# Kernel optimization log

Hardware: AMD Instinct MI355X
Metric: run time of the kernel (lower is better)

Reference implementation:

```python
import jax, jax.numpy as jnp
import numpy as np

S, R, STEPS, EPS = 1, 1, 4, 1e-6

def setup_inputs() -> dict:
    key = jax.random.key(0)
    k1, k2, k3, k4 = jax.random.split(key, 4)
    x = jax.random.normal(k1, (8, 16, 160, 48, 48), dtype=jnp.float32)
    W_pre = jax.random.normal(k2, (8, 16), dtype=jnp.float32) * 0.1   # align conv 1x1x1
    W_post1 = jax.random.normal(k3, (8, 8), dtype=jnp.float32) * 0.1
    W_post2 = jax.random.normal(k4, (16, 8), dtype=jnp.float32) * 0.1
    return {"x": x, "W_pre": W_pre, "W_post1": W_post1, "W_post2": W_post2}

def _update_coef(x3, bases, coef):
    # x3:[B,D,N] bases:[B,D,R] coef:[B,N,R] -- NMF multiplicative coef update
    num = jnp.einsum('bdn,bdr->bnr', x3, bases)
    btb = jnp.einsum('bdr,bdq->brq', bases, bases)
    den = jnp.einsum('bnr,brq->bnq', coef, btb)
    return coef * num / (den + EPS)

def _local_step(x3, bases, coef):
    coef = _update_coef(x3, bases, coef)
    num = jnp.einsum('bdn,bnr->bdr', x3, coef)
    ctc = jnp.einsum('bnr,bnq->brq', coef, coef)
    den = jnp.einsum('bdr,brq->bdq', bases, ctc)
    bases = bases * num / (den + EPS)
    return bases, coef

def _nmf(x3):
    # rand_init bases = normalize(ones, dim=1) = 1/sqrt(D)
    B, D, N = x3.shape
    bases = jnp.full((B, D, R), 1.0 / np.sqrt(float(D)), dtype=x3.dtype)
    def _infer(x3, bases):
        coef = jax.nn.softmax(jnp.einsum('bdn,bdr->bnr', x3, bases), axis=-1)  # inv_t = 1
        for _ in range(STEPS):
            bases, coef = _local_step(x3, bases, coef)
        return bases, coef
    # torch runs local_inference under no_grad
    bases, coef = jax.lax.stop_gradient(_infer(x3, bases))
    coef = _update_coef(x3, bases, coef)  # compute_coef (differentiable)
    return jnp.einsum('bdr,bnr->bdn', bases, coef)  # reconstruction [B,D,N]

def reference(x, W_pre, W_post1, W_post2):
    B, C, T, H, W = x.shape
    # pre 1x1x1 conv (no bias) + ReLU
    h = jax.nn.relu(jnp.einsum('oc,bcthw->bothw', W_pre, x))
    Ca = W_pre.shape[0]
    D, N = T // S, Ca * H * W
    x3 = h.reshape(B * S, D, N)  # flat view, matches torch .view on contiguous [B,Ca,T,H,W]
    recon = _nmf(x3).reshape(B, Ca, T, H, W)
    # post: 1x1x1 conv + ReLU, then 1x1x1 conv (no act)
    y = jax.nn.relu(jnp.einsum('oc,bcthw->bothw', W_post1, recon))
    y = jnp.einsum('oc,bcthw->bothw', W_post2, y)
    return y
```

## Files before the change

### kernel.cpp

```cpp
#include <hip/hip_runtime.h>
#include <math.h>

using u16 = unsigned short;
using u32 = unsigned int;

typedef __attribute__((ext_vector_type(8))) short bf16x8;
typedef __attribute__((ext_vector_type(16))) float f32x16;

constexpr int Bn  = 8;
constexpr int Cin = 16;
constexpr int Tn  = 160;
constexpr int HWn = 2304;
constexpr int Dn  = 160;
constexpr int Nn  = 8 * HWn;
constexpr int PB  = Dn * Nn;
constexpr int PLANE4 = Tn * HWn / 4;
constexpr float EPSF = 1e-6f;
constexpr float B0F  = 0.07905694150420949f;
constexpr float BTB0 = 160.0f * B0F * B0F;

constexpr int NSPLIT = 72;
constexpr int NTRI   = 15;
constexpr int TSZ    = NTRI * 1024;
constexpr int GD     = Dn * Dn;

constexpr size_t G_OFF  = (size_t)Bn * PB / 2;
constexpr size_t GP_OFF = G_OFF + (size_t)Bn * GD;

constexpr int OFF_COEF = 0;
constexpr int OFF_B4   = Bn * Nn;
constexpr int OFF_BTB  = OFF_B4 + Bn * Dn;

__device__ inline float bf2f(u16 u) { return __uint_as_float(((u32)u) << 16); }
__device__ inline u16 f2bf(float f) {
    u32 x = __float_as_uint(f);
    return (u16)((x + 0x7fffu + ((x >> 16) & 1u)) >> 16);
}

__device__ inline void tri_pair(int t, int& a, int& bb) {
    a = (t >= 14) ? 4 : (t >= 12) ? 3 : (t >= 9) ? 2 : (t >= 5) ? 1 : 0;
    int base = (a == 0) ? 0 : (a == 1) ? 5 : (a == 2) ? 9 : (a == 3) ? 12 : 14;
    bb = a + (t - base);
}

__global__ __launch_bounds__(256) void k_pre(const float* __restrict__ x,
                                             const float* __restrict__ Wpre,
                                             u16* __restrict__ h) {
    __shared__ float Ws[8 * Cin];
    if (threadIdx.x < 8 * Cin) Ws[threadIdx.x] = Wpre[threadIdx.x];
    __syncthreads();
    int gid = blockIdx.x * 256 + threadIdx.x;
    int b   = gid / PLANE4;
    int pos = gid - b * PLANE4;
    const float4* xb = reinterpret_cast<const float4*>(x) + (size_t)(b * Cin) * PLANE4 + pos;
    float4 acc[8];
#pragma unroll
    for (int o = 0; o < 8; ++o) acc[o] = make_float4(0.f, 0.f, 0.f, 0.f);
#pragma unroll
    for (int c = 0; c < Cin; ++c) {
        float4 xv = xb[(size_t)c * PLANE4];
#pragma unroll
        for (int o = 0; o < 8; ++o) {
            float w = Ws[o * Cin + c];
            acc[o].x = fmaf(w, xv.x, acc[o].x);
            acc[o].y = fmaf(w, xv.y, acc[o].y);
            acc[o].z = fmaf(w, xv.z, acc[o].z);
            acc[o].w = fmaf(w, xv.w, acc[o].w);
        }
    }
#pragma unroll
    for (int o = 0; o < 8; ++o) {
        float4 v = acc[o];
        u32 w0 = (u32)f2bf(fmaxf(v.x, 0.f)) | ((u32)f2bf(fmaxf(v.y, 0.f)) << 16);
        u32 w1 = (u32)f2bf(fmaxf(v.z, 0.f)) | ((u32)f2bf(fmaxf(v.w, 0.f)) << 16);
        uint2* dst = reinterpret_cast<uint2*>(h + (size_t)(b * 8 + o) * (Tn * HWn)) + pos;
        *dst = make_uint2(w0, w1);
    }
}

__global__ __launch_bounds__(256, 3) void k_gram(const u16* __restrict__ h,
                                                 float* __restrict__ Gpart) {
    __shared__ uint4 tile[Dn * 16];
    const int blk = blockIdx.x;
    const int b = blk / NSPLIT, s = blk - b * NSPLIT;
    const int tid = threadIdx.x;
    const int w = tid >> 6, l = tid & 63, lo = l & 31, hi = l >> 5;
    const int c8 = tid & 15, rg = tid >> 4;
    const int swl = lo & 7;

    int a0, b0_, a1, b1_, a2, b2_, a3, b3_;
    tri_pair(w,      a0, b0_);
    tri_pair(w + 4,  a1, b1_);
    tri_pair(w + 8,  a2, b2_);
    const bool has3 = (w < 3);
    tri_pair(has3 ? (w + 12) : 0, a3, b3_);
    const int rA0 = a0 * 32, rB0 = b0_ * 32, dg0 = (a0 == b0_);
    const int rA1 = a1 * 32, rB1 = b1_ * 32, dg1 = (a1 == b1_);
    const int rA2 = a2 * 32, rB2 = b2_ * 32, dg2 = (a2 == b2_);
    const int rA3 = a3 * 32, rB3 = b3_ * 32, dg3 = (a3 == b3_);

    f32x16 acc0, acc1, acc2, acc3;
#pragma unroll
    for (int q = 0; q < 16; ++q) { acc0[q] = 0.f; acc1[q] = 0.f; acc2[q] = 0.f; acc3[q] = 0.f; }

    const u16* hb = h + (size_t)b * PB;
#pragma unroll 1
    for (int cc = 0; cc < 2; ++cc) {
        const int kbase = (s * 2 + cc) * 128;
        __syncthreads();
#pragma unroll
        for (int k = 0; k < 10; ++k) {
            int row = rg + 16 * k;
            uint4 v = *reinterpret_cast<const uint4*>(
                hb + (size_t)row * Nn + kbase + c8 * 8);
            tile[row * 16 + (c8 ^ (row & 7))] = v;
        }
        __syncthreads();
#pragma unroll
        for (int kk = 0; kk < 8; ++kk) {
            const int sw = (kk * 2 + hi) ^ swl;
            bf16x8 fa0 = __builtin_bit_cast(bf16x8, tile[(rA0 + lo) * 16 + sw]);
            bf16x8 fb0 = dg0 ? fa0 : __builtin_bit_cast(bf16x8, tile[(rB0 + lo) * 16 + sw]);
            acc0 = __builtin_amdgcn_mfma_f32_32x32x16_bf16(fa0, fb0, acc0, 0, 0, 0);
            bf16x8 fa1 = __builtin_bit_cast(bf16x8, tile[(rA1 + lo) * 16 + sw]);
            bf16x8 fb1 = dg1 ? fa1 : __builtin_bit_cast(bf16x8, tile[(rB1 + lo) * 16 + sw]);
            acc1 = __builtin_amdgcn_mfma_f32_32x32x16_bf16(fa1, fb1, acc1, 0, 0, 0);
            bf16x8 fa2 = __builtin_bit_cast(bf16x8, tile[(rA2 + lo) * 16 + sw]);
            bf16x8 fb2 = dg2 ? fa2 : __builtin_bit_cast(bf16x8, tile[(rB2 + lo) * 16 + sw]);
            acc2 = __builtin_amdgcn_mfma_f32_32x32x16_bf16(fa2, fb2, acc2, 0, 0, 0);
            if (has3) {
                bf16x8 fa3 = __builtin_bit_cast(bf16x8, tile[(rA3 + lo) * 16 + sw]);
                bf16x8 fb3 = dg3 ? fa3 : __builtin_bit_cast(bf16x8, tile[(rB3 + lo) * 16 + sw]);
                acc3 = __builtin_amdgcn_mfma_f32_32x32x16_bf16(fa3, fb3, acc3, 0, 0, 0);
            }
        }
    }

    float* Gp = Gpart + (size_t)blk * TSZ;
#pragma unroll
    for (int q = 0; q < 16; ++q) {
        int row = ((q & 3) + 8 * (q >> 2) + 4 * hi) * 32 + lo;
        Gp[(w)      * 1024 + row] = acc0[q];
        Gp[(w + 4)  * 1024 + row] = acc1[q];
        Gp[(w + 8)  * 1024 + row] = acc2[q];
        if (has3) Gp[(w + 12) * 1024 + row] = acc3[q];
    }
}

__global__ __launch_bounds__(256) void k_redG(const float* __restrict__ Gpart,
                                              float* __restrict__ G) {
    int idx = blockIdx.x * 256 + threadIdx.x;
    int b = idx / TSZ;
    int r = idx - b * TSZ;
    int t = r >> 10;
    int e = r & 1023;
    int er = e >> 5, ec = e & 31;
    int a, bb;
    tri_pair(t, a, bb);
    const float* gp = Gpart + (size_t)(b * NSPLIT) * TSZ + r;
    float s = 0.f;
#pragma unroll 8
    for (int k = 0; k < NSPLIT; ++k) s += gp[(size_t)k * TSZ];
    float* Gb = G + (size_t)b * GD;
    int i = a * 32 + er, j = bb * 32 + ec;
    Gb[i * Dn + j] = s;
    Gb[j * Dn + i] = s;
}

__global__ __launch_bounds__(192) void k_chainB(const float* __restrict__ G,
                                                float* __restrict__ bases4,
                                                float* __restrict__ btb4) {
    __shared__ float bS[Dn];
    __shared__ float uS[Dn];
    __shared__ float sc[2];
    const int b = blockIdx.x;
    const int tid = threadIdx.x;
    const float* Gb = G + (size_t)b * GD;

    if (tid < Dn) bS[tid] = B0F;
    __syncthreads();

    float btb = BTB0;
#pragma unroll 1
    for (int j = 1; j <= 4; ++j) {
        if (tid < Dn) {
            float s = 0.f;
            const float* row = Gb + tid * Dn;
#pragma unroll 8
            for (int d = 0; d < Dn; ++d) s = fmaf(row[d], bS[d], s);
            uS[tid] = s;
        }
        __syncthreads();
        if (tid == 0) {
            float bgb = 0.f;
            for (int d = 0; d < Dn; ++d) bgb = fmaf(bS[d], uS[d], bgb);
            sc[0] = bgb;
        }
        __syncthreads();
        float denom = (j == 1) ? (btb + EPSF) : btb;
        float ctc = sc[0] / (denom * denom);
        float inv = 1.f / (denom * ctc);
        if (tid < Dn) bS[tid] = uS[tid] * inv;
        __syncthreads();
        if (tid == 0) {
            float ss = 0.f;
            for (int d = 0; d < Dn; ++d) ss = fmaf(bS[d], bS[d], ss);
            sc[1] = ss;
        }
        __syncthreads();
        btb = sc[1];
    }
    if (tid < Dn) bases4[b * Dn + tid] = bS[tid];
    if (tid == 0) btb4[b] = btb;
}

__global__ __launch_bounds__(256, 3) void k_coef5(
        const u16* __restrict__ h, float* __restrict__ coef,
        const float* __restrict__ bases4, const float* __restrict__ btb4)
{
    __shared__ float bsS[Dn];
    __shared__ float partA[4][128];
    const int blk = blockIdx.x;
    const int b   = blk / 144;
    const int cb  = blk - b * 144;
    const int colbase = cb * 128;
    const int tid = threadIdx.x, c8 = tid & 15, rg = tid >> 4;

    if (tid < Dn) bsS[tid] = bases4[b * Dn + tid] / btb4[b];
    __syncthreads();

    const u16* hp = h + (size_t)b * PB + colbase + c8 * 8;
    float acc[8];
#pragma unroll
    for (int j = 0; j < 8; ++j) acc[j] = 0.f;
#pragma unroll
    for (int k = 0; k < 10; ++k) {
        uint4 v = *reinterpret_cast<const uint4*>(hp + (size_t)(rg + 16 * k) * Nn);
        float w = bsS[rg + 16 * k];
        u32 vv[4] = { v.x, v.y, v.z, v.w };
#pragma unroll
        for (int q = 0; q < 4; ++q) {
            acc[2*q]   = fmaf(w, bf2f((u16)(vv[q] & 0xffffu)), acc[2*q]);
            acc[2*q+1] = fmaf(w, bf2f((u16)(vv[q] >> 16)),     acc[2*q+1]);
        }
    }
#pragma unroll
    for (int j = 0; j < 8; ++j) {
        acc[j] += __shfl_xor(acc[j], 16, 64);
        acc[j] += __shfl_xor(acc[j], 32, 64);
    }
    if ((tid & 48) == 0) {
        int w = tid >> 6;
#pragma unroll
        for (int j = 0; j < 8; ++j) partA[w][c8 * 8 + j] = acc[j];
    }
    __syncthreads();

    if (tid < 128)
        coef[(size_t)b * Nn + colbase + tid] =
            partA[0][tid] + partA[1][tid] + partA[2][tid] + partA[3][tid];
}

__global__ __launch_bounds__(192) void k_post(const float* __restrict__ coef,
                                              const float* __restrict__ bases,
                                              const float* __restrict__ Wp1,
                                              const float* __restrict__ Wp2,
                                              float* __restrict__ out) {
    int b = blockIdx.x / Tn;
    int t = blockIdx.x - b * Tn;
    int tau = t >> 3;
    float u[8];
#pragma unroll
    for (int p = 0; p < 8; ++p) {
        float s = 0.f;
#pragma unroll
        for (int ca = 0; ca < 8; ++ca)
            s = fmaf(Wp1[p * 8 + ca], bases[b * Dn + ca * 20 + tau], s);
        u[p] = fmaxf(s, 0.f);
    }
    float v[16];
#pragma unroll
    for (int o = 0; o < 16; ++o) {
        float s = 0.f;
#pragma unroll
        for (int p = 0; p < 8; ++p) s = fmaf(Wp2[o * 8 + p], u[p], s);
        v[o] = s;
    }
    const float4* c4 = reinterpret_cast<const float4*>(coef + (size_t)b * Nn + (t & 7) * HWn);
    float4* o4 = reinterpret_cast<float4*>(out) + (size_t)(b * 16 * Tn + t) * (HWn / 4);
#pragma unroll
    for (int it = 0; it < 3; ++it) {
        int p4 = threadIdx.x + it * 192;
        float4 cv = c4[p4];
#pragma unroll
        for (int o = 0; o < 16; ++o) {
            float4 ov = make_float4(cv.x * v[o], cv.y * v[o], cv.z * v[o], cv.w * v[o]);
            o4[(size_t)o * (Tn * (HWn / 4)) + p4] = ov;
        }
    }
}

extern "C" void kernel_launch(void* const* d_in, const int* in_sizes, int n_in,
                              void* d_out, int out_size, void* d_ws, size_t ws_size,
                              hipStream_t stream) {
    const float* x    = (const float*)d_in[0];
    const float* Wpre = (const float*)d_in[1];
    const float* Wp1  = (const float*)d_in[2];
    const float* Wp2  = (const float*)d_in[3];
    float* out = (float*)d_out;

    u16*   h     = (u16*)d_out;
    float* G     = out + G_OFF;
    float* Gpart = out + GP_OFF;
    float* ws = (float*)d_ws;
    float* coef   = ws + OFF_COEF;
    float* bases4 = ws + OFF_B4;
    float* btb4   = ws + OFF_BTB;

    k_pre<<<Bn * PLANE4 / 256, 256, 0, stream>>>(x, Wpre, h);
    k_gram<<<Bn * NSPLIT, 256, 0, stream>>>(h, Gpart);
    k_redG<<<Bn * TSZ / 256, 256, 0, stream>>>(Gpart, G);
    k_chainB<<<Bn, 192, 0, stream>>>(G, bases4, btb4);
    k_coef5<<<Bn * 144, 256, 0, stream>>>(h, coef, bases4, btb4);
    k_post<<<Bn * Tn, 192, 0, stream>>>(coef, bases4, Wp1, Wp2, out);
}
```

Before: 146.0 us.

## Fuse pre-conv into Gram kernel, computing bf16 tiles directly from x

```diff
diff --git a/kernel.cpp b/kernel.cpp
--- a/kernel.cpp
+++ b/kernel.cpp
@@ -14,12 +14,12 @@
 constexpr int Dn  = 160;
 constexpr int Nn  = 8 * HWn;
 constexpr int PB  = Dn * Nn;
-constexpr int PLANE4 = Tn * HWn / 4;
+constexpr int TH  = Tn * HWn;
 constexpr float EPSF = 1e-6f;
 constexpr float B0F  = 0.07905694150420949f;
 constexpr float BTB0 = 160.0f * B0F * B0F;
 
-constexpr int NSPLIT = 72;
+constexpr int NSPLIT = 36;
 constexpr int NTRI   = 15;
 constexpr int TSZ    = NTRI * 1024;
 constexpr int GD     = Dn * Dn;
@@ -43,50 +43,20 @@
     bb = a + (t - base);
 }
 
-__global__ __launch_bounds__(256) void k_pre(const float* __restrict__ x,
-                                             const float* __restrict__ Wpre,
-                                             u16* __restrict__ h) {
+__global__ __launch_bounds__(256, 2) void k_pregram(
+        const float* __restrict__ x, const float* __restrict__ Wpre,
+        u16* __restrict__ h, float* __restrict__ Gpart) {
+    __shared__ uint4 tile[Dn * 16];
     __shared__ float Ws[8 * Cin];
-    if (threadIdx.x < 8 * Cin) Ws[threadIdx.x] = Wpre[threadIdx.x];
-    __syncthreads();
-    int gid = blockIdx.x * 256 + threadIdx.x;
-    int b   = gid / PLANE4;
-    int pos = gid - b * PLANE4;
-    const float4* xb = reinterpret_cast<const float4*>(x) + (size_t)(b * Cin) * PLANE4 + pos;
-    float4 acc[8];
-#pragma unroll
-    for (int o = 0; o < 8; ++o) acc[o] = make_float4(0.f, 0.f, 0.f, 0.f);
-#pragma unroll
-    for (int c = 0; c < Cin; ++c) {
-        float4 xv = xb[(size_t)c * PLANE4];
-#pragma unroll
-        for (int o = 0; o < 8; ++o) {
-            float w = Ws[o * Cin + c];
-            acc[o].x = fmaf(w, xv.x, acc[o].x);
-            acc[o].y = fmaf(w, xv.y, acc[o].y);
-            acc[o].z = fmaf(w, xv.z, acc[o].z);
-            acc[o].w = fmaf(w, xv.w, acc[o].w);
-        }
-    }
-#pragma unroll
-    for (int o = 0; o < 8; ++o) {
-        float4 v = acc[o];
-        u32 w0 = (u32)f2bf(fmaxf(v.x, 0.f)) | ((u32)f2bf(fmaxf(v.y, 0.f)) << 16);
-        u32 w1 = (u32)f2bf(fmaxf(v.z, 0.f)) | ((u32)f2bf(fmaxf(v.w, 0.f)) << 16);
-        uint2* dst = reinterpret_cast<uint2*>(h + (size_t)(b * 8 + o) * (Tn * HWn)) + pos;
-        *dst = make_uint2(w0, w1);
-    }
-}
-
-__global__ __launch_bounds__(256, 3) void k_gram(const u16* __restrict__ h,
-                                                 float* __restrict__ Gpart) {
-    __shared__ uint4 tile[Dn * 16];
     const int blk = blockIdx.x;
     const int b = blk / NSPLIT, s = blk - b * NSPLIT;
     const int tid = threadIdx.x;
     const int w = tid >> 6, l = tid & 63, lo = l & 31, hi = l >> 5;
-    const int c8 = tid & 15, rg = tid >> 4;
     const int swl = lo & 7;
+    const int cp  = tid & 63;
+    const int tg5 = (tid >> 6) * 5;
+
+    if (tid < 8 * Cin) Ws[tid] = Wpre[tid];
 
     int a0, b0_, a1, b1_, a2, b2_, a3, b3_;
     tri_pair(w,      a0, b0_);
@@ -103,19 +73,57 @@
 #pragma unroll
     for (int q = 0; q < 16; ++q) { acc0[q] = 0.f; acc1[q] = 0.f; acc2[q] = 0.f; acc3[q] = 0.f; }
 
-    const u16* hb = h + (size_t)b * PB;
+    const float* xb = x + (size_t)b * Cin * TH;
+    u16* hb = h + (size_t)b * PB;
+    u32* tw = reinterpret_cast<u32*>(tile);
+    __syncthreads();
+
 #pragma unroll 1
-    for (int cc = 0; cc < 2; ++cc) {
-        const int kbase = (s * 2 + cc) * 128;
-        __syncthreads();
-#pragma unroll
-        for (int k = 0; k < 10; ++k) {
-            int row = rg + 16 * k;
-            uint4 v = *reinterpret_cast<const uint4*>(
-                hb + (size_t)row * Nn + kbase + c8 * 8);
-            tile[row * 16 + (c8 ^ (row & 7))] = v;
-        }
-        __syncthreads();
+    for (int cc = 0; cc < 4; ++cc) {
+        const int kbase = s * 512 + cc * 128;
+        const int r = kbase / HWn;
+        const int hw0 = kbase - r * HWn + 2 * cp;
+        const float* xp = xb + (size_t)r * HWn + hw0;
+
+        float ac[5][16];
+#pragma unroll
+        for (int i = 0; i < 5; ++i)
+#pragma unroll
+            for (int q = 0; q < 16; ++q) ac[i][q] = 0.f;
+
+#pragma unroll 2
+        for (int c = 0; c < Cin; ++c) {
+            float2 xv[5];
+#pragma unroll
+            for (int i = 0; i < 5; ++i)
+                xv[i] = *reinterpret_cast<const float2*>(
+                    xp + (size_t)c * TH + (size_t)((tg5 + i) * 8) * HWn);
+#pragma unroll
+            for (int ca = 0; ca < 8; ++ca) {
+                float wv = Ws[ca * Cin + c];
+#pragma unroll
+                for (int i = 0; i < 5; ++i) {
+                    ac[i][2 * ca]     = fmaf(wv, xv[i].x, ac[i][2 * ca]);
+                    ac[i][2 * ca + 1] = fmaf(wv, xv[i].y, ac[i][2 * ca + 1]);
+                }
+            }
+        }
+
+        __syncthreads();
+#pragma unroll
+        for (int ca = 0; ca < 8; ++ca) {
+#pragma unroll
+            for (int i = 0; i < 5; ++i) {
+                int d = ca * 20 + tg5 + i;
+                u32 pkd = (u32)f2bf(fmaxf(ac[i][2 * ca], 0.f))
+                        | ((u32)f2bf(fmaxf(ac[i][2 * ca + 1], 0.f)) << 16);
+                tw[d * 64 + (((cp >> 2) ^ (d & 7)) << 2) + (cp & 3)] = pkd;
+                *reinterpret_cast<u32*>(hb + (size_t)d * Nn + kbase + 2 * cp) = pkd;
+            }
+        }
+        __syncthreads();
+        __builtin_amdgcn_sched_barrier(0);
+
 #pragma unroll
         for (int kk = 0; kk < 8; ++kk) {
             const int sw = (kk * 2 + hi) ^ swl;
@@ -134,6 +142,7 @@
                 acc3 = __builtin_amdgcn_mfma_f32_32x32x16_bf16(fa3, fb3, acc3, 0, 0, 0);
             }
         }
+        __syncthreads();
     }
 
     float* Gp = Gpart + (size_t)blk * TSZ;
@@ -159,7 +168,7 @@
     tri_pair(t, a, bb);
     const float* gp = Gpart + (size_t)(b * NSPLIT) * TSZ + r;
     float s = 0.f;
-#pragma unroll 8
+#pragma unroll 4
     for (int k = 0; k < NSPLIT; ++k) s += gp[(size_t)k * TSZ];
     float* Gb = G + (size_t)b * GD;
     int i = a * 32 + er, j = bb * 32 + ec;
@@ -317,8 +326,7 @@
     float* bases4 = ws + OFF_B4;
     float* btb4   = ws + OFF_BTB;
 
-    k_pre<<<Bn * PLANE4 / 256, 256, 0, stream>>>(x, Wpre, h);
-    k_gram<<<Bn * NSPLIT, 256, 0, stream>>>(h, Gpart);
+    k_pregram<<<Bn * NSPLIT, 256, 0, stream>>>(x, Wpre, h, Gpart);
     k_redG<<<Bn * TSZ / 256, 256, 0, stream>>>(Gpart, G);
     k_chainB<<<Bn, 192, 0, stream>>>(G, bases4, btb4);
     k_coef5<<<Bn * 144, 256, 0, stream>>>(h, coef, bases4, btb4);
```

Measured after the change: 267.7 us. 83.3% more time.

## Replace Gram partial buffer and reduction kernel with atomic accumulation

Applied to the files above, without the earlier changes.

```diff
diff --git a/kernel.cpp b/kernel.cpp
--- a/kernel.cpp
+++ b/kernel.cpp
@@ -21,11 +21,9 @@
 
 constexpr int NSPLIT = 72;
 constexpr int NTRI   = 15;
-constexpr int TSZ    = NTRI * 1024;
 constexpr int GD     = Dn * Dn;
 
 constexpr size_t G_OFF  = (size_t)Bn * PB / 2;
-constexpr size_t GP_OFF = G_OFF + (size_t)Bn * GD;
 
 constexpr int OFF_COEF = 0;
 constexpr int OFF_B4   = Bn * Nn;
@@ -45,11 +43,15 @@
 
 __global__ __launch_bounds__(256) void k_pre(const float* __restrict__ x,
                                              const float* __restrict__ Wpre,
-                                             u16* __restrict__ h) {
+                                             u16* __restrict__ h,
+                                             float* __restrict__ G) {
     __shared__ float Ws[8 * Cin];
     if (threadIdx.x < 8 * Cin) Ws[threadIdx.x] = Wpre[threadIdx.x];
     __syncthreads();
     int gid = blockIdx.x * 256 + threadIdx.x;
+    if (gid < Bn * GD / 4) {
+        reinterpret_cast<float4*>(G)[gid] = make_float4(0.f, 0.f, 0.f, 0.f);
+    }
     int b   = gid / PLANE4;
     int pos = gid - b * PLANE4;
     const float4* xb = reinterpret_cast<const float4*>(x) + (size_t)(b * Cin) * PLANE4 + pos;
@@ -79,7 +81,7 @@
 }
 
 __global__ __launch_bounds__(256, 3) void k_gram(const u16* __restrict__ h,
-                                                 float* __restrict__ Gpart) {
+                                                 float* __restrict__ G) {
     __shared__ uint4 tile[Dn * 16];
     const int blk = blockIdx.x;
     const int b = blk / NSPLIT, s = blk - b * NSPLIT;
@@ -136,35 +138,15 @@
         }
     }
 
-    float* Gp = Gpart + (size_t)blk * TSZ;
+    float* Gb = G + (size_t)b * GD;
 #pragma unroll
     for (int q = 0; q < 16; ++q) {
-        int row = ((q & 3) + 8 * (q >> 2) + 4 * hi) * 32 + lo;
-        Gp[(w)      * 1024 + row] = acc0[q];
-        Gp[(w + 4)  * 1024 + row] = acc1[q];
-        Gp[(w + 8)  * 1024 + row] = acc2[q];
-        if (has3) Gp[(w + 12) * 1024 + row] = acc3[q];
-    }
-}
-
-__global__ __launch_bounds__(256) void k_redG(const float* __restrict__ Gpart,
-                                              float* __restrict__ G) {
-    int idx = blockIdx.x * 256 + threadIdx.x;
-    int b = idx / TSZ;
-    int r = idx - b * TSZ;
-    int t = r >> 10;
-    int e = r & 1023;
-    int er = e >> 5, ec = e & 31;
-    int a, bb;
-    tri_pair(t, a, bb);
-    const float* gp = Gpart + (size_t)(b * NSPLIT) * TSZ + r;
-    float s = 0.f;
-#pragma unroll 8
-    for (int k = 0; k < NSPLIT; ++k) s += gp[(size_t)k * TSZ];
-    float* Gb = G + (size_t)b * GD;
-    int i = a * 32 + er, j = bb * 32 + ec;
-    Gb[i * Dn + j] = s;
-    Gb[j * Dn + i] = s;
+        int R = (q & 3) + 8 * (q >> 2) + 4 * hi;
+        atomicAdd(&Gb[(a0 * 32 + R) * Dn + b0_ * 32 + lo], acc0[q]);
+        atomicAdd(&Gb[(a1 * 32 + R) * Dn + b1_ * 32 + lo], acc1[q]);
+        atomicAdd(&Gb[(a2 * 32 + R) * Dn + b2_ * 32 + lo], acc2[q]);
+        if (has3) atomicAdd(&Gb[(a3 * 32 + R) * Dn + b3_ * 32 + lo], acc3[q]);
+    }
 }
 
 __global__ __launch_bounds__(192) void k_chainB(const float* __restrict__ G,
@@ -185,9 +167,11 @@
     for (int j = 1; j <= 4; ++j) {
         if (tid < Dn) {
             float s = 0.f;
-            const float* row = Gb + tid * Dn;
 #pragma unroll 8
-            for (int d = 0; d < Dn; ++d) s = fmaf(row[d], bS[d], s);
+            for (int d = 0; d < Dn; ++d) {
+                float g = (tid <= d) ? Gb[tid * Dn + d] : Gb[d * Dn + tid];
+                s = fmaf(g, bS[d], s);
+            }
             uS[tid] = s;
         }
         __syncthreads();
@@ -311,15 +295,13 @@
 
     u16*   h     = (u16*)d_out;
     float* G     = out + G_OFF;
-    float* Gpart = out + GP_OFF;
     float* ws = (float*)d_ws;
     float* coef   = ws + OFF_COEF;
     float* bases4 = ws + OFF_B4;
     float* btb4   = ws + OFF_BTB;
 
-    k_pre<<<Bn * PLANE4 / 256, 256, 0, stream>>>(x, Wpre, h);
-    k_gram<<<Bn * NSPLIT, 256, 0, stream>>>(h, Gpart);
-    k_redG<<<Bn * TSZ / 256, 256, 0, stream>>>(Gpart, G);
+    k_pre<<<Bn * PLANE4 / 256, 256, 0, stream>>>(x, Wpre, h, G);
+    k_gram<<<Bn * NSPLIT, 256, 0, stream>>>(h, G);
     k_chainB<<<Bn, 192, 0, stream>>>(G, bases4, btb4);
     k_coef5<<<Bn * 144, 256, 0, stream>>>(h, coef, bases4, btb4);
     k_post<<<Bn * Tn, 192, 0, stream>>>(coef, bases4, Wp1, Wp2, out);
```

After: 199.3 us. +36.5%, slower.

## Fuse coefficient computation with post convs, moving h to workspace

Applied to the files above, without the earlier changes.

```diff
diff --git a/kernel.cpp b/kernel.cpp
--- a/kernel.cpp
+++ b/kernel.cpp
@@ -27,9 +27,11 @@
 constexpr size_t G_OFF  = (size_t)Bn * PB / 2;
 constexpr size_t GP_OFF = G_OFF + (size_t)Bn * GD;
 
-constexpr int OFF_COEF = 0;
-constexpr int OFF_B4   = Bn * Nn;
+constexpr int OFF_B4   = 0;
 constexpr int OFF_BTB  = OFF_B4 + Bn * Dn;
+constexpr int OFF_COEF = 2048;
+constexpr size_t OFF_H = 151552;
+constexpr size_t WS_NEED_A = (OFF_H + (size_t)Bn * PB / 2) * 4;
 
 __device__ inline float bf2f(u16 u) { return __uint_as_float(((u32)u) << 16); }
 __device__ inline u16 f2bf(float f) {
@@ -300,6 +302,89 @@
     }
 }
 
+__global__ __launch_bounds__(256, 3) void k_cpost(
+        const u16* __restrict__ h,
+        const float* __restrict__ bases4, const float* __restrict__ btb4,
+        const float* __restrict__ Wp1, const float* __restrict__ Wp2,
+        float* __restrict__ out)
+{
+    __shared__ float bsS[Dn];
+    __shared__ float partA[4][128];
+    __shared__ float uS[160];
+    __shared__ float vS[320];
+    __shared__ float cS[128];
+    const int blk = blockIdx.x;
+    const int b   = blk / 144;
+    const int cb  = blk - b * 144;
+    const int colbase = cb * 128;
+    const int r   = cb / 18;
+    const int hw0 = (cb - r * 18) * 128;
+    const int tid = threadIdx.x, c8 = tid & 15, rg = tid >> 4;
+
+    if (tid < Dn) bsS[tid] = bases4[b * Dn + tid] / btb4[b];
+    if (tid < 160) {
+        int p = tid / 20, tau = tid - p * 20;
+        float s = 0.f;
+#pragma unroll
+        for (int ca = 0; ca < 8; ++ca)
+            s = fmaf(Wp1[p * 8 + ca], bases4[b * Dn + ca * 20 + tau], s);
+        uS[tid] = fmaxf(s, 0.f);
+    }
+    __syncthreads();
+
+    for (int i = tid; i < 320; i += 256) {
+        int o = i / 20, tau = i - o * 20;
+        float s = 0.f;
+#pragma unroll
+        for (int p = 0; p < 8; ++p) s = fmaf(Wp2[o * 8 + p], uS[p * 20 + tau], s);
+        vS[i] = s;
+    }
+
+    const u16* hp = h + (size_t)b * PB + colbase + c8 * 8;
+    float acc[8];
+#pragma unroll
+    for (int j = 0; j < 8; ++j) acc[j] = 0.f;
+#pragma unroll
+    for (int k = 0; k < 10; ++k) {
+        uint4 v = *reinterpret_cast<const uint4*>(hp + (size_t)(rg + 16 * k) * Nn);
+        float w = bsS[rg + 16 * k];
+        u32 vv[4] = { v.x, v.y, v.z, v.w };
+#pragma unroll
+        for (int q = 0; q < 4; ++q) {
+            acc[2*q]   = fmaf(w, bf2f((u16)(vv[q] & 0xffffu)), acc[2*q]);
+            acc[2*q+1] = fmaf(w, bf2f((u16)(vv[q] >> 16)),     acc[2*q+1]);
+        }
+    }
+#pragma unroll
+    for (int j = 0; j < 8; ++j) {
+        acc[j] += __shfl_xor(acc[j], 16, 64);
+        acc[j] += __shfl_xor(acc[j], 32, 64);
+    }
+    if ((tid & 48) == 0) {
+        int w = tid >> 6;
+#pragma unroll
+        for (int j = 0; j < 8; ++j) partA[w][c8 * 8 + j] = acc[j];
+    }
+    __syncthreads();
+    if (tid < 128)
+        cS[tid] = partA[0][tid] + partA[1][tid] + partA[2][tid] + partA[3][tid];
+    __syncthreads();
+
+    const int col4 = tid & 31;
+    const int rbase = tid >> 5;
+    float4 c = *reinterpret_cast<const float4*>(&cS[col4 * 4]);
+    float4* o4 = reinterpret_cast<float4*>(out);
+    const size_t base_b = (size_t)(b * 16) * 160 * 576 + (size_t)r * 576 + (hw0 >> 2) + col4;
+#pragma unroll 8
+    for (int k = 0; k < 40; ++k) {
+        int row = rbase + 8 * k;
+        int o = row / 20, tau = row - o * 20;
+        float vv = vS[row];
+        o4[base_b + (size_t)(o * 160 + tau * 8) * 576] =
+            make_float4(c.x * vv, c.y * vv, c.z * vv, c.w * vv);
+    }
+}
+
 extern "C" void kernel_launch(void* const* d_in, const int* in_sizes, int n_in,
                               void* d_out, int out_size, void* d_ws, size_t ws_size,
                               hipStream_t stream) {
@@ -308,19 +393,28 @@
     const float* Wp1  = (const float*)d_in[2];
     const float* Wp2  = (const float*)d_in[3];
     float* out = (float*)d_out;
-
-    u16*   h     = (u16*)d_out;
-    float* G     = out + G_OFF;
-    float* Gpart = out + GP_OFF;
-    float* ws = (float*)d_ws;
-    float* coef   = ws + OFF_COEF;
+    float* ws  = (float*)d_ws;
+
+    float* G      = out + G_OFF;
+    float* Gpart  = out + GP_OFF;
     float* bases4 = ws + OFF_B4;
     float* btb4   = ws + OFF_BTB;
 
-    k_pre<<<Bn * PLANE4 / 256, 256, 0, stream>>>(x, Wpre, h);
-    k_gram<<<Bn * NSPLIT, 256, 0, stream>>>(h, Gpart);
-    k_redG<<<Bn * TSZ / 256, 256, 0, stream>>>(Gpart, G);
-    k_chainB<<<Bn, 192, 0, stream>>>(G, bases4, btb4);
-    k_coef5<<<Bn * 144, 256, 0, stream>>>(h, coef, bases4, btb4);
-    k_post<<<Bn * Tn, 192, 0, stream>>>(coef, bases4, Wp1, Wp2, out);
-}
+    if (ws_size >= WS_NEED_A) {
+        u16* h = (u16*)(ws + OFF_H);
+        k_pre<<<Bn * PLANE4 / 256, 256, 0, stream>>>(x, Wpre, h);
+        k_gram<<<Bn * NSPLIT, 256, 0, stream>>>(h, Gpart);
+        k_redG<<<Bn * TSZ / 256, 256, 0, stream>>>(Gpart, G);
+        k_chainB<<<Bn, 192, 0, stream>>>(G, bases4, btb4);
+        k_cpost<<<Bn * 144, 256, 0, stream>>>(h, bases4, btb4, Wp1, Wp2, out);
+    } else {
+        u16*   h    = (u16*)d_out;
+        float* coef = ws + OFF_COEF;
+        k_pre<<<Bn * PLANE4 / 256, 256, 0, stream>>>(x, Wpre, h);
+        k_gram<<<Bn * NSPLIT, 256, 0, stream>>>(h, Gpart);
+        k_redG<<<Bn * TSZ / 256, 256, 0, stream>>>(Gpart, G);
+        k_chainB<<<Bn, 192, 0, stream>>>(G, bases4, btb4);
+        k_coef5<<<Bn * 144, 256, 0, stream>>>(h, coef, bases4, btb4);
+        k_post<<<Bn * Tn, 192, 0, stream>>>(coef, bases4, Wp1, Wp2, out);
+    }
+}
```

Result: slower. 172.1 us (+17.9%).
